# Kernel optimization log

Hardware: AMD Instinct MI355X
Metric: run time of the kernel (lower is better)

The kernel has to match this reference:

```python
import jax, jax.numpy as jnp
import numpy as np

N = 20000
E = 640000
IN_CH = 256
HID = 128
OUT_CH = 64
HEADS = 8
C1 = HID // HEADS   # 16 per-head dim, layer 1 (concat)
C2 = OUT_CH         # 64 per-head dim, layer 2 (head mean)
NEG_SLOPE = 0.2


def gat_conv(x, edge_index, W, a_src, a_dst, b, concat):
    """PyG GATConv (no self loops, eval mode / no dropout).
    W: [F_in, H*C], a_src/a_dst: [H, C], b: [H*C] or [C]."""
    H, C = a_src.shape
    h = (x @ W).reshape(-1, H, C)                      # [N, H, C]
    s_src = jnp.einsum('nhc,hc->nh', h, a_src)         # [N, H]
    s_dst = jnp.einsum('nhc,hc->nh', h, a_dst)         # [N, H]
    src, dst = edge_index[0], edge_index[1]
    e = jax.nn.leaky_relu(s_src[src] + s_dst[dst], NEG_SLOPE)  # [E, H]
    # segment softmax over incoming edges of each destination node
    m = jax.ops.segment_max(e, dst, num_segments=N)    # [N, H] (-inf for isolated)
    p = jnp.exp(e - m[dst])                            # [E, H]
    z = jax.ops.segment_sum(p, dst, num_segments=N)    # [N, H]
    alpha = p / z[dst]                                 # [E, H]
    out = jax.ops.segment_sum(h[src] * alpha[..., None], dst, num_segments=N)  # [N,H,C]
    out = out.reshape(-1, H * C) if concat else out.mean(axis=1)
    return out + b


def hetero_layer(x, edge_indices, Ws, a_srcs, a_dsts, bs, concat):
    # HeteroConv(aggr='mean') over edge types targeting 'user'
    outs = [gat_conv(x, edge_indices[t], Ws[t], a_srcs[t], a_dsts[t], bs[t], concat)
            for t in range(len(edge_indices))]
    return sum(outs) / len(outs)


def setup_inputs() -> dict:
    key = jax.random.key(0)
    ks = jax.random.split(key, 16)
    g = 0.1
    return {
        'x': jax.random.normal(ks[0], (N, IN_CH), dtype=jnp.float32),
        'edge_index_a': jax.random.randint(ks[1], (2, E), 0, N, dtype=jnp.int32).astype(jnp.int64),
        'edge_index_b': jax.random.randint(ks[2], (2, E), 0, N, dtype=jnp.int32).astype(jnp.int64),
        # layer 1 params, stacked over 2 edge types
        'W1': jax.random.normal(ks[3], (2, IN_CH, HEADS * C1), dtype=jnp.float32) * g,
        'a1_src': jax.random.normal(ks[4], (2, HEADS, C1), dtype=jnp.float32) * g,
        'a1_dst': jax.random.normal(ks[5], (2, HEADS, C1), dtype=jnp.float32) * g,
        'b1': jnp.zeros((2, HEADS * C1), dtype=jnp.float32),
        # layer 2 params
        'W2': jax.random.normal(ks[6], (2, HID, HEADS * C2), dtype=jnp.float32) * g,
        'a2_src': jax.random.normal(ks[7], (2, HEADS, C2), dtype=jnp.float32) * g,
        'a2_dst': jax.random.normal(ks[8], (2, HEADS, C2), dtype=jnp.float32) * g,
        'b2': jnp.zeros((2, C2), dtype=jnp.float32),
        # classifier
        'Wc1': jax.random.normal(ks[9], (OUT_CH, 32), dtype=jnp.float32) * g,
        'bc1': jnp.zeros((32,), dtype=jnp.float32),
        'Wc2': jax.random.normal(ks[10], (32, 2), dtype=jnp.float32) * g,
        'bc2': jnp.zeros((2,), dtype=jnp.float32),
    }


def reference(x, edge_index_a, edge_index_b, W1, a1_src, a1_dst, b1,
              W2, a2_src, a2_dst, b2, Wc1, bc1, Wc2, bc2):
    eis = [edge_index_a, edge_index_b]
    h = hetero_layer(x, eis, W1, a1_src, a1_dst, b1, concat=True)   # [N, 128]
    h = jax.nn.elu(h)  # (dropout is identity in eval mode)
    h = hetero_layer(h, eis, W2, a2_src, a2_dst, b2, concat=False)  # [N, 64]
    h = jax.nn.elu(h)
    logits = jax.nn.relu(h @ Wc1 + bc1) @ Wc2 + bc2                 # [N, 2]
    return logits
```

## Files before the change

### kernel.cpp

```cpp
#include <hip/hip_runtime.h>
#include <hip/hip_bf16.h>
#include <math.h>

#define NN 20000
#define EE 640000
#define NB 157
#define BCAP 5120
#define NBLK 160
#define CHNK 4000

typedef float v2f __attribute__((ext_vector_type(2)));
typedef __attribute__((ext_vector_type(8))) short bf16x8;
typedef __attribute__((ext_vector_type(4))) float f32x4;

__device__ __forceinline__ void wave_fence() {
  __builtin_amdgcn_wave_barrier();
  asm volatile("s_waitcnt lgkmcnt(0)" ::: "memory");
  __builtin_amdgcn_wave_barrier();
}

__device__ __forceinline__ unsigned pack_bf2(float a, float b) {
  __hip_bfloat162 h2 = __float22bfloat162_rn(make_float2(a, b));
  return *(unsigned*)&h2;
}
__device__ __forceinline__ float2 unpack_bf2(unsigned v) {
  float2 r;
  unsigned lo = v << 16, hi = v & 0xffff0000u;
  r.x = __uint_as_float(lo);
  r.y = __uint_as_float(hi);
  return r;
}

__global__ __launch_bounds__(256) void bin_k(const int* __restrict__ ea,
                                             const int* __restrict__ eb,
                                             int* __restrict__ gcnt,
                                             int* __restrict__ bbuf) {
  int t = blockIdx.y;
  const int* ei = t ? eb : ea;
  int tid = threadIdx.x;
  __shared__ int lh[NB], lbase[NB];
  if (tid < NB) lh[tid] = 0;
  __syncthreads();
  int e0 = blockIdx.x * CHNK;
  int e1 = min(e0 + CHNK, EE);
  int myb[16], myr[16], myv[16];
#pragma unroll
  for (int i = 0; i < 16; ++i) {
    int e = e0 + tid + i * 256;
    if (e < e1) {
      int s = ei[e], d = ei[EE + e];
      int b = d >> 7;
      myb[i] = b;
      myv[i] = (s << 7) | (d & 127);
      myr[i] = atomicAdd(&lh[b], 1);
    } else {
      myb[i] = -1;
    }
  }
  __syncthreads();
  if (tid < NB) {
    int c = lh[tid];
    lbase[tid] = c ? atomicAdd(&gcnt[t * NB + tid], c) : 0;
  }
  __syncthreads();
#pragma unroll
  for (int i = 0; i < 16; ++i) {
    int b = myb[i];
    if (b >= 0) {
      int pos = lbase[b] + myr[i];
      if (pos < BCAP) bbuf[((size_t)t * NB + b) * BCAP + pos] = myv[i];
    }
  }
}

__global__ __launch_bounds__(512) void bscan_k(const int* __restrict__ gcnt,
                                               int* __restrict__ bstart) {
  __shared__ int buf[512];
  int tid = threadIdx.x;
  int t = tid >> 8, b = tid & 255;
  int val = (b < NB) ? gcnt[t * NB + b] : 0;
  buf[tid] = val;
  __syncthreads();
  for (int s = 1; s < 256; s <<= 1) {
    int x = ((tid & 255) >= s) ? buf[tid - s] : 0;
    __syncthreads();
    buf[tid] += x;
    __syncthreads();
  }
  if (b < NB) bstart[t * NB + b] = buf[tid] - val;
}

__global__ __launch_bounds__(256) void build_k(const int* __restrict__ gcnt,
                                               const int* __restrict__ bstart,
                                               const int* __restrict__ bbuf,
                                               int* __restrict__ rowptr,
                                               int* __restrict__ csr) {
  int b = blockIdx.x, t = blockIdx.y;
  int cnt = gcnt[t * NB + b];
  int start = bstart[t * NB + b];
  int n0 = b << 7;
  int nlocal = min(128, NN - n0);
  int tid = threadIdx.x;
  __shared__ int arr[128], lcur[128];
  if (tid < 128) arr[tid] = 0;
  __syncthreads();
  const int* ebuf = bbuf + ((size_t)t * NB + b) * BCAP;
  for (int i = tid; i < cnt; i += 256) atomicAdd(&arr[ebuf[i] & 127], 1);
  __syncthreads();
  int deg = (tid < 128) ? arr[tid] : 0;
  for (int s = 1; s < 128; s <<= 1) {
    int x = (tid < 128 && tid >= s) ? arr[tid - s] : 0;
    __syncthreads();
    if (tid < 128) arr[tid] += x;
    __syncthreads();
  }
  if (tid < nlocal) {
    int incl = arr[tid];
    rowptr[t * (NN + 1) + n0 + tid + 1] = start + incl;
    lcur[tid] = start + incl - deg;
  }
  if (b == 0 && tid == 0) rowptr[t * (NN + 1)] = 0;
  __syncthreads();
  for (int i = tid; i < cnt; i += 256) {
    int v = ebuf[i];
    int pos = atomicAdd(&lcur[v & 127], 1);
    csr[(size_t)t * EE + pos] = v >> 7;
  }
}

__global__ void packx_k(const float* __restrict__ x, unsigned* __restrict__ Xp) {
  int idx = blockIdx.x * 256 + threadIdx.x;
  if (idx >= NN * 128) return;
  float2 f = *(const float2*)&x[(size_t)idx * 2];
  Xp[idx] = pack_bf2(f.x, f.y);
}

__global__ void foldBT1_k(const float* __restrict__ W1, unsigned* __restrict__ BT1) {
  int idx = blockIdx.x * 256 + threadIdx.x;
  if (idx >= 32768) return;
  int t = idx >> 14, r = idx & 16383, c = r >> 7, kw = r & 127;
  float v0 = W1[(size_t)t * 32768 + (size_t)(2 * kw) * 128 + c];
  float v1 = W1[(size_t)t * 32768 + (size_t)(2 * kw + 1) * 128 + c];
  BT1[idx] = pack_bf2(v0, v1);
}

__global__ __launch_bounds__(256) void gemm1_k(const unsigned* __restrict__ Xp,
                                               const unsigned* __restrict__ BT1,
                                               unsigned* __restrict__ h1b) {
  int tid = threadIdx.x, w = tid >> 6, l = tid & 63;
  int lr = l & 15, lg = l >> 4;
  int rowbase = blockIdx.x * 64 + w * 16;
  int arow = rowbase + lr;
  if (arow > NN - 1) arow = NN - 1;
  f32x4 acc[2][8];
#pragma unroll
  for (int t = 0; t < 2; ++t)
#pragma unroll
    for (int ct = 0; ct < 8; ++ct) acc[t][ct] = (f32x4){0.f, 0.f, 0.f, 0.f};
  const unsigned* ap = Xp + (size_t)arow * 128 + lg * 4;
#pragma unroll
  for (int kw = 0; kw < 128; kw += 16) {
    uint4 av = *(const uint4*)(ap + kw);
    bf16x8 af = *(const bf16x8*)&av;
#pragma unroll
    for (int t = 0; t < 2; ++t) {
#pragma unroll
      for (int ct = 0; ct < 8; ++ct) {
        uint4 bv = *(const uint4*)(BT1 + (size_t)t * 16384 + (size_t)(ct * 16 + lr) * 128 + lg * 4 + kw);
        acc[t][ct] = __builtin_amdgcn_mfma_f32_16x16x32_bf16(af, *(const bf16x8*)&bv, acc[t][ct], 0, 0, 0);
      }
    }
  }
  bool wr = (l & 1) == 0;
#pragma unroll
  for (int t = 0; t < 2; ++t) {
#pragma unroll
    for (int ct = 0; ct < 8; ++ct) {
      int col = ct * 16 + lr;
#pragma unroll
      for (int r = 0; r < 4; ++r) {
        float v = acc[t][ct][r];
        float v2 = __shfl_xor(v, 1);
        int row = rowbase + lg * 4 + r;
        if (wr && row < NN)
          h1b[(size_t)t * NN * 64 + (size_t)row * 64 + (col >> 1)] = pack_bf2(v, v2);
      }
    }
  }
}

__global__ void scoreb_k(const unsigned* __restrict__ hb, const float* __restrict__ as_,
                         const float* __restrict__ ad_, float* __restrict__ ss,
                         float* __restrict__ sd) {
  int idx = blockIdx.x * 256 + threadIdx.x;
  if (idx >= 2 * NN * 8) return;
  int t = idx / (NN * 8), r = idx % (NN * 8), n = r / 8, hh = r % 8;
  const unsigned* hrow = hb + (size_t)t * NN * 64 + (size_t)n * 64 + hh * 8;
  const float* a1 = as_ + t * 128 + hh * 16;
  const float* a2 = ad_ + t * 128 + hh * 16;
  uint4 u0 = *(const uint4*)&hrow[0];
  uint4 u1 = *(const uint4*)&hrow[4];
  unsigned uu[8] = {u0.x, u0.y, u0.z, u0.w, u1.x, u1.y, u1.z, u1.w};
  float s1 = 0.f, s2 = 0.f;
#pragma unroll
  for (int q = 0; q < 8; ++q) {
    float2 f = unpack_bf2(uu[q]);
    s1 += f.x * a1[2 * q] + f.y * a1[2 * q + 1];
    s2 += f.x * a2[2 * q] + f.y * a2[2 * q + 1];
  }
  ss[idx] = s1; sd[idx] = s2;
}

__device__ __forceinline__ float lrelu(float v) { return v > 0.f ? v : 0.2f * v; }

__global__ __launch_bounds__(256) void aggw1_k(const int* __restrict__ rowptr,
                                               const int* __restrict__ csr,
                                               const float* __restrict__ ssrc,
                                               const float* __restrict__ sdst,
                                               const unsigned* __restrict__ hb,
                                               unsigned* __restrict__ out) {
  int t = blockIdx.y;
  rowptr += t * (NN + 1); csr += (size_t)t * EE;
  ssrc += (size_t)t * NN * 8; sdst += (size_t)t * NN * 8;
  hb += (size_t)t * NN * 64; out += (size_t)t * NN * 64;
  int tid = threadIdx.x, w = tid >> 6, lane = tid & 63;
  int n = blockIdx.x * 4 + w;
  int row = rowptr[n], end = rowptr[n + 1];
  __shared__ __align__(16) int sidx[4][64];
  __shared__ __align__(16) float sexp[4][64][8];
  float4 sda = *(const float4*)&sdst[(size_t)n * 8];
  float4 sdb = *(const float4*)&sdst[(size_t)n * 8 + 4];
  float za_x = 0.f, za_y = 0.f, za_z = 0.f, za_w = 0.f;
  float zb_x = 0.f, zb_y = 0.f, zb_z = 0.f, zb_w = 0.f;
  int hme = lane >> 3;
  unsigned lane4 = lane << 2;
  const char* hbc = (const char*)hb;
  v2f acc = {0.f, 0.f};
  for (int base = row; base < end; base += 64) {
    int cnt = min(64, end - base);
    if (lane < cnt) {
      int s = csr[base + lane];
      sidx[w][lane] = s << 8;
      float4 pa = *(const float4*)&ssrc[(size_t)s * 8];
      float4 pb = *(const float4*)&ssrc[(size_t)s * 8 + 4];
      float4 ea, eb;
      ea.x = __expf(lrelu(pa.x + sda.x)); ea.y = __expf(lrelu(pa.y + sda.y));
      ea.z = __expf(lrelu(pa.z + sda.z)); ea.w = __expf(lrelu(pa.w + sda.w));
      eb.x = __expf(lrelu(pb.x + sdb.x)); eb.y = __expf(lrelu(pb.y + sdb.y));
      eb.z = __expf(lrelu(pb.z + sdb.z)); eb.w = __expf(lrelu(pb.w + sdb.w));
      za_x += ea.x; za_y += ea.y; za_z += ea.z; za_w += ea.w;
      zb_x += eb.x; zb_y += eb.y; zb_z += eb.z; zb_w += eb.w;
      *(float4*)&sexp[w][lane][0] = ea;
      *(float4*)&sexp[w][lane][4] = eb;
    }
    wave_fence();
    int g = 0;
    for (; g + 8 <= cnt; g += 8) {
      unsigned off[8];
      *(int4*)&off[0] = *(const int4*)&sidx[w][g];
      *(int4*)&off[4] = *(const int4*)&sidx[w][g + 4];
      unsigned uv[8];
#pragma unroll
      for (int j = 0; j < 8; ++j)
        uv[j] = *(const unsigned*)(hbc + (off[j] | lane4));
#pragma unroll
      for (int j = 0; j < 8; ++j) {
        float a = sexp[w][g + j][hme];
        float2 vf = unpack_bf2(uv[j]);
        v2f v = {vf.x, vf.y};
        acc += a * v;
      }
    }
    for (; g < cnt; ++g) {
      unsigned off = (unsigned)sidx[w][g];
      unsigned uvr = *(const unsigned*)(hbc + (off | lane4));
      float a = sexp[w][g][hme];
      float2 vf = unpack_bf2(uvr);
      v2f v = {vf.x, vf.y};
      acc += a * v;
    }
    wave_fence();
  }
#pragma unroll
  for (int off = 32; off; off >>= 1) {
    za_x += __shfl_xor(za_x, off); za_y += __shfl_xor(za_y, off);
    za_z += __shfl_xor(za_z, off); za_w += __shfl_xor(za_w, off);
    zb_x += __shfl_xor(zb_x, off); zb_y += __shfl_xor(zb_y, off);
    zb_z += __shfl_xor(zb_z, off); zb_w += __shfl_xor(zb_w, off);
  }
  float zh[8] = {za_x, za_y, za_z, za_w, zb_x, zb_y, zb_z, zb_w};
  float z = zh[hme];
  float iz = z > 0.f ? 1.f / z : 0.f;
  out[(size_t)n * 64 + lane] = pack_bf2(acc.x * iz, acc.y * iz);
}

__global__ void combine1_k(const unsigned* __restrict__ oa, const unsigned* __restrict__ ob,
                           const float* __restrict__ b1, unsigned* __restrict__ hmidb) {
  int idx = blockIdx.x * 256 + threadIdx.x;
  if (idx >= NN * 64) return;
  int j2 = idx & 63, j = j2 * 2;
  float2 va = unpack_bf2(oa[idx]);
  float2 vb = unpack_bf2(ob[idx]);
  float vx = 0.5f * ((va.x + b1[j]) + (vb.x + b1[128 + j]));
  float vy = 0.5f * ((va.y + b1[j + 1]) + (vb.y + b1[128 + j + 1]));
  vx = vx > 0.f ? vx : (__expf(vx) - 1.f);
  vy = vy > 0.f ? vy : (__expf(vy) - 1.f);
  hmidb[idx] = pack_bf2(vx, vy);
}

__global__ void fold2_k(const float* __restrict__ W2, const float* __restrict__ a2s,
                        const float* __restrict__ a2d, float* __restrict__ wsf,
                        float* __restrict__ wdf) {
  int idx = blockIdx.x * 256 + threadIdx.x;
  if (idx >= 2048) return;
  int t = idx >> 10, r = idx & 1023, hh = r >> 7, k = r & 127;
  const float* wrow = W2 + (size_t)t * 65536 + (size_t)k * 512 + hh * 64;
  const float* as = a2s + t * 512 + hh * 64;
  const float* ad = a2d + t * 512 + hh * 64;
  float s1 = 0.f, s2 = 0.f;
  for (int c = 0; c < 64; ++c) { s1 += wrow[c] * as[c]; s2 += wrow[c] * ad[c]; }
  wsf[idx] = s1; wdf[idx] = s2;
}

__global__ void foldBT_k(const float* __restrict__ W2, unsigned* __restrict__ BTp) {
  int idx = blockIdx.x * 256 + threadIdx.x;
  if (idx >= 65536) return;
  int t = idx >> 15, r = idx & 32767, c = r >> 9, kw = r & 511;
  int K0 = kw * 2, K1 = K0 + 1;
  int hh0 = K0 >> 7, kk0 = K0 & 127;
  int hh1 = K1 >> 7, kk1 = K1 & 127;
  float v0 = 0.125f * W2[(size_t)t * 65536 + (size_t)kk0 * 512 + hh0 * 64 + c];
  float v1 = 0.125f * W2[(size_t)t * 65536 + (size_t)kk1 * 512 + hh1 * 64 + c];
  BTp[idx] = pack_bf2(v0, v1);
}

__global__ void score2_k(const unsigned* __restrict__ hmidb, const float* __restrict__ wsf,
                         const float* __restrict__ wdf, float* __restrict__ ss,
                         float* __restrict__ sdo) {
  int idx = blockIdx.x * 256 + threadIdx.x;
  if (idx >= NN * 8) return;
  int n = idx >> 3, hh = idx & 7;
  const unsigned* hm = hmidb + (size_t)n * 64;
  const float* w0s = wsf + (size_t)hh * 128;
  const float* w0d = wdf + (size_t)hh * 128;
  const float* w1s = wsf + (size_t)(8 + hh) * 128;
  const float* w1d = wdf + (size_t)(8 + hh) * 128;
  float s0s = 0.f, s0d = 0.f, s1s = 0.f, s1d = 0.f;
#pragma unroll 4
  for (int q = 0; q < 64; ++q) {
    float2 f = unpack_bf2(hm[q]);
    int c = 2 * q;
    s0s += f.x * w0s[c] + f.y * w0s[c + 1];
    s0d += f.x * w0d[c] + f.y * w0d[c + 1];
    s1s += f.x * w1s[c] + f.y * w1s[c + 1];
    s1d += f.x * w1d[c] + f.y * w1d[c + 1];
  }
  ss[idx] = s0s; sdo[idx] = s0d;
  ss[NN * 8 + idx] = s1s; sdo[NN * 8 + idx] = s1d;
}

__global__ __launch_bounds__(256) void aggw2_k(const int* __restrict__ rowptr,
                                               const int* __restrict__ csr,
                                               const float* __restrict__ ssrc,
                                               const float* __restrict__ sdst,
                                               const unsigned* __restrict__ hmidb,
                                               unsigned* __restrict__ aggp) {
  int t = blockIdx.y;
  rowptr += t * (NN + 1); csr += (size_t)t * EE;
  ssrc += (size_t)t * NN * 8; sdst += (size_t)t * NN * 8;
  aggp += (size_t)t * NN * 512;
  int tid = threadIdx.x, w = tid >> 6, lane = tid & 63;
  int n = blockIdx.x * 4 + w;
  int row = rowptr[n], end = rowptr[n + 1];
  __shared__ __align__(16) int sidx[4][64];
  __shared__ __align__(16) float sexp[4][64][8];
  float4 sda = *(const float4*)&sdst[(size_t)n * 8];
  float4 sdb = *(const float4*)&sdst[(size_t)n * 8 + 4];
  float za_x = 0.f, za_y = 0.f, za_z = 0.f, za_w = 0.f;
  float zb_x = 0.f, zb_y = 0.f, zb_z = 0.f, zb_w = 0.f;
  unsigned lane4 = lane << 2;
  const char* hbc = (const char*)hmidb;
  v2f acc[8];
#pragma unroll
  for (int i = 0; i < 8; ++i) acc[i] = (v2f){0.f, 0.f};
  for (int base = row; base < end; base += 64) {
    int cnt = min(64, end - base);
    if (lane < cnt) {
      int s = csr[base + lane];
      sidx[w][lane] = s << 8;
      float4 pa = *(const float4*)&ssrc[(size_t)s * 8];
      float4 pb = *(const float4*)&ssrc[(size_t)s * 8 + 4];
      float4 ea, eb;
      ea.x = __expf(lrelu(pa.x + sda.x)); ea.y = __expf(lrelu(pa.y + sda.y));
      ea.z = __expf(lrelu(pa.z + sda.z)); ea.w = __expf(lrelu(pa.w + sda.w));
      eb.x = __expf(lrelu(pb.x + sdb.x)); eb.y = __expf(lrelu(pb.y + sdb.y));
      eb.z = __expf(lrelu(pb.z + sdb.z)); eb.w = __expf(lrelu(pb.w + sdb.w));
      za_x += ea.x; za_y += ea.y; za_z += ea.z; za_w += ea.w;
      zb_x += eb.x; zb_y += eb.y; zb_z += eb.z; zb_w += eb.w;
      *(float4*)&sexp[w][lane][0] = ea;
      *(float4*)&sexp[w][lane][4] = eb;
    }
    wave_fence();
    int g = 0;
    for (; g + 8 <= cnt; g += 8) {
      unsigned off[8];
      *(int4*)&off[0] = *(const int4*)&sidx[w][g];
      *(int4*)&off[4] = *(const int4*)&sidx[w][g + 4];
      unsigned uv[8];
#pragma unroll
      for (int j = 0; j < 8; ++j)
        uv[j] = *(const unsigned*)(hbc + (off[j] | lane4));
#pragma unroll
      for (int j = 0; j < 8; ++j) {
        float4 ea = *(const float4*)&sexp[w][g + j][0];
        float4 eb = *(const float4*)&sexp[w][g + j][4];
        float2 vf = unpack_bf2(uv[j]);
        v2f v = {vf.x, vf.y};
        acc[0] += ea.x * v;
        acc[1] += ea.y * v;
        acc[2] += ea.z * v;
        acc[3] += ea.w * v;
        acc[4] += eb.x * v;
        acc[5] += eb.y * v;
        acc[6] += eb.z * v;
        acc[7] += eb.w * v;
      }
    }
    for (; g < cnt; ++g) {
      unsigned off = (unsigned)sidx[w][g];
      unsigned uvr = *(const unsigned*)(hbc + (off | lane4));
      float4 ea = *(const float4*)&sexp[w][g][0];
      float4 eb = *(const float4*)&sexp[w][g][4];
      float2 vf = unpack_bf2(uvr);
      v2f v = {vf.x, vf.y};
      acc[0] += ea.x * v;
      acc[1] += ea.y * v;
      acc[2] += ea.z * v;
      acc[3] += ea.w * v;
      acc[4] += eb.x * v;
      acc[5] += eb.y * v;
      acc[6] += eb.z * v;
      acc[7] += eb.w * v;
    }
    wave_fence();
  }
#pragma unroll
  for (int off = 32; off; off >>= 1) {
    za_x += __shfl_xor(za_x, off); za_y += __shfl_xor(za_y, off);
    za_z += __shfl_xor(za_z, off); za_w += __shfl_xor(za_w, off);
    zb_x += __shfl_xor(zb_x, off); zb_y += __shfl_xor(zb_y, off);
    zb_z += __shfl_xor(zb_z, off); zb_w += __shfl_xor(zb_w, off);
  }
  float zh[8] = {za_x, za_y, za_z, za_w, zb_x, zb_y, zb_z, zb_w};
#pragma unroll
  for (int i = 0; i < 8; ++i) {
    float z = zh[i];
    float iz = z > 0.f ? 1.f / z : 0.f;
    aggp[(size_t)n * 512 + i * 64 + lane] = pack_bf2(acc[i].x * iz, acc[i].y * iz);
  }
}

__global__ __launch_bounds__(256) void gemm2_k(const unsigned* __restrict__ Ap,
                                               const unsigned* __restrict__ BT,
                                               const float* __restrict__ b2,
                                               float* __restrict__ feat) {
  int tid = threadIdx.x, w = tid >> 6, l = tid & 63;
  int lr = l & 15, lgq = l >> 4;
  int rowbase = blockIdx.x * 64 + w * 16;
  int arow = rowbase + lr;
  if (arow > NN - 1) arow = NN - 1;
  f32x4 acc0 = {0.f, 0.f, 0.f, 0.f}, acc1 = acc0, acc2 = acc0, acc3 = acc0;
#pragma unroll
  for (int t = 0; t < 2; ++t) {
    const unsigned* ap = Ap + (size_t)t * NN * 512 + (size_t)arow * 512 + lgq * 4;
    const unsigned* bp = BT + t * 32768 + lr * 512 + lgq * 4;
    for (int kw = 0; kw < 512; kw += 16) {
      uint4 av = *(const uint4*)(ap + kw);
      uint4 bv0 = *(const uint4*)(bp + kw);
      uint4 bv1 = *(const uint4*)(bp + 16 * 512 + kw);
      uint4 bv2 = *(const uint4*)(bp + 32 * 512 + kw);
      uint4 bv3 = *(const uint4*)(bp + 48 * 512 + kw);
      bf16x8 afq = *(const bf16x8*)&av;
      acc0 = __builtin_amdgcn_mfma_f32_16x16x32_bf16(afq, *(const bf16x8*)&bv0, acc0, 0, 0, 0);
      acc1 = __builtin_amdgcn_mfma_f32_16x16x32_bf16(afq, *(const bf16x8*)&bv1, acc1, 0, 0, 0);
      acc2 = __builtin_amdgcn_mfma_f32_16x16x32_bf16(afq, *(const bf16x8*)&bv2, acc2, 0, 0, 0);
      acc3 = __builtin_amdgcn_mfma_f32_16x16x32_bf16(afq, *(const bf16x8*)&bv3, acc3, 0, 0, 0);
    }
  }
  f32x4 accs[4] = {acc0, acc1, acc2, acc3};
#pragma unroll
  for (int ct = 0; ct < 4; ++ct) {
    int col = ct * 16 + lr;
    float bsum = b2[col] + b2[64 + col];
#pragma unroll
    for (int r = 0; r < 4; ++r) {
      int rowq = rowbase + lgq * 4 + r;
      if (rowq < NN) {
        float v = 0.5f * (accs[ct][r] + bsum);
        v = v > 0.f ? v : (__expf(v) - 1.f);
        feat[(size_t)rowq * 64 + col] = v;
      }
    }
  }
}

__global__ __launch_bounds__(256) void cls_k(const float* __restrict__ feat,
                                             const float* __restrict__ Wc1,
                                             const float* __restrict__ bc1,
                                             const float* __restrict__ Wc2,
                                             const float* __restrict__ bc2,
                                             float* __restrict__ out) {
  __shared__ float w1[64 * 32];
  __shared__ float w2[64];
  __shared__ float b1s[32], b2s[2];
  __shared__ float fs[8 * 64];
  __shared__ float hs[8 * 32];
  int tid = threadIdx.x;
  for (int i = tid; i < 2048; i += 256) w1[i] = Wc1[i];
  if (tid < 64) w2[tid] = Wc2[tid];
  if (tid < 32) b1s[tid] = bc1[tid];
  if (tid < 2) b2s[tid] = bc2[tid];
  int nbase = blockIdx.x * 8;
  for (int i = tid; i < 512; i += 256) fs[i] = feat[(size_t)nbase * 64 + i];
  __syncthreads();
  int local = tid >> 5, tt = tid & 31;
  const float* f = fs + local * 64;
  float acc = b1s[tt];
#pragma unroll
  for (int c = 0; c < 64; ++c) acc += f[c] * w1[c * 32 + tt];
  hs[local * 32 + tt] = fmaxf(acc, 0.f);
  __syncthreads();
  if (tid < 16) {
    int l = tid >> 1, j = tid & 1;
    float o = b2s[j];
#pragma unroll
    for (int i = 0; i < 32; ++i) o += hs[l * 32 + i] * w2[i * 2 + j];
    out[(size_t)(nbase + l) * 2 + j] = o;
  }
}

extern "C" void kernel_launch(void* const* d_in, const int* in_sizes, int n_in,
                              void* d_out, int out_size, void* d_ws, size_t ws_size,
                              hipStream_t stream) {
  const float* x   = (const float*)d_in[0];
  const int* eia   = (const int*)d_in[1];
  const int* eib   = (const int*)d_in[2];
  const float* W1  = (const float*)d_in[3];
  const float* a1s = (const float*)d_in[4];
  const float* a1d = (const float*)d_in[5];
  const float* b1  = (const float*)d_in[6];
  const float* W2  = (const float*)d_in[7];
  const float* a2s = (const float*)d_in[8];
  const float* a2d = (const float*)d_in[9];
  const float* b2  = (const float*)d_in[10];
  const float* Wc1 = (const float*)d_in[11];
  const float* bc1 = (const float*)d_in[12];
  const float* Wc2 = (const float*)d_in[13];
  const float* bc2 = (const float*)d_in[14];
  float* out = (float*)d_out;

  char* ws = (char*)d_ws;
  size_t off = 0;
  auto alloc = [&](size_t bytes) -> char* {
    char* p = ws + off;
    off += (bytes + 255) & ~(size_t)255;
    return p;
  };
  int* gcnt       = (int*)alloc((size_t)2 * NB * 4);
  int* bstart     = (int*)alloc((size_t)2 * NB * 4);
  int* bbuf       = (int*)alloc((size_t)2 * NB * BCAP * 4);
  int* rowptr     = (int*)alloc((size_t)2 * (NN + 1) * 4);
  int* csr        = (int*)alloc((size_t)2 * EE * 4);
  unsigned* Xp    = (unsigned*)alloc((size_t)NN * 128 * 4);
  unsigned* BT1   = (unsigned*)alloc((size_t)32768 * 4);
  unsigned* h1b   = (unsigned*)alloc((size_t)2 * NN * 64 * 4);
  float* s1s      = (float*)alloc((size_t)2 * NN * 8 * 4);
  float* s1d      = (float*)alloc((size_t)2 * NN * 8 * 4);
  unsigned* o1p   = (unsigned*)alloc((size_t)2 * NN * 64 * 4);
  unsigned* hmidb = (unsigned*)alloc((size_t)NN * 64 * 4);
  float* wsf      = (float*)alloc((size_t)2048 * 4);
  float* wdf      = (float*)alloc((size_t)2048 * 4);
  unsigned* BTp   = (unsigned*)alloc((size_t)65536 * 4);
  float* s2s      = (float*)alloc((size_t)2 * NN * 8 * 4);
  float* s2d      = (float*)alloc((size_t)2 * NN * 8 * 4);
  unsigned* aggp  = (unsigned*)alloc((size_t)2 * NN * 512 * 4);
  float* feat     = (float*)alloc((size_t)NN * 64 * 4);

  hipMemsetAsync(gcnt, 0, (size_t)2 * NB * 4, stream);
  bin_k<<<dim3(NBLK, 2), 256, 0, stream>>>(eia, eib, gcnt, bbuf);
  bscan_k<<<1, 512, 0, stream>>>(gcnt, bstart);
  build_k<<<dim3(NB, 2), 256, 0, stream>>>(gcnt, bstart, bbuf, rowptr, csr);

  fold2_k<<<8, 256, 0, stream>>>(W2, a2s, a2d, wsf, wdf);
  foldBT_k<<<256, 256, 0, stream>>>(W2, BTp);
  foldBT1_k<<<128, 256, 0, stream>>>(W1, BT1);
  packx_k<<<(NN * 128 + 255) / 256, 256, 0, stream>>>(x, Xp);

  gemm1_k<<<(NN + 63) / 64, 256, 0, stream>>>(Xp, BT1, h1b);
  scoreb_k<<<(2 * NN * 8 + 255) / 256, 256, 0, stream>>>(h1b, a1s, a1d, s1s, s1d);
  aggw1_k<<<dim3(NN / 4, 2), 256, 0, stream>>>(rowptr, csr, s1s, s1d, h1b, o1p);
  combine1_k<<<(NN * 64 + 255) / 256, 256, 0, stream>>>(o1p, o1p + (size_t)NN * 64, b1, hmidb);

  score2_k<<<(NN * 8 + 255) / 256, 256, 0, stream>>>(hmidb, wsf, wdf, s2s, s2d);
  aggw2_k<<<dim3(NN / 4, 2), 256, 0, stream>>>(rowptr, csr, s2s, s2d, hmidb, aggp);
  gemm2_k<<<(NN + 63) / 64, 256, 0, stream>>>(aggp, BTp, b2, feat);

  cls_k<<<NN / 8, 256, 0, stream>>>(feat, Wc1, bc1, Wc2, bc2, out);
}
```

Before: 435.4 us.

## Replace bucketed CSR build with global-atomic degree count, scan, and scatter

```diff
diff --git a/kernel.cpp b/kernel.cpp
--- a/kernel.cpp
+++ b/kernel.cpp
@@ -4,10 +4,6 @@
 
 #define NN 20000
 #define EE 640000
-#define NB 157
-#define BCAP 5120
-#define NBLK 160
-#define CHNK 4000
 
 typedef float v2f __attribute__((ext_vector_type(2)));
 typedef __attribute__((ext_vector_type(8))) short bf16x8;
@@ -31,100 +27,64 @@
   return r;
 }
 
-__global__ __launch_bounds__(256) void bin_k(const int* __restrict__ ea,
-                                             const int* __restrict__ eb,
-                                             int* __restrict__ gcnt,
-                                             int* __restrict__ bbuf) {
+__global__ __launch_bounds__(256) void degcnt_k(const int* __restrict__ ea,
+                                                const int* __restrict__ eb,
+                                                int* __restrict__ deg) {
   int t = blockIdx.y;
   const int* ei = t ? eb : ea;
+  int* dg = deg + t * NN;
+  for (int e = blockIdx.x * 256 + threadIdx.x; e < EE; e += gridDim.x * 256)
+    atomicAdd(&dg[ei[EE + e]], 1);
+}
+
+__global__ __launch_bounds__(1024) void scan_k(const int* __restrict__ deg,
+                                               int* __restrict__ rowptr,
+                                               int* __restrict__ cur) {
+  int t = blockIdx.x;
+  const int* d = deg + t * NN;
+  int* rp = rowptr + t * (NN + 1);
+  int* cu = cur + t * NN;
+  __shared__ int part[1024];
   int tid = threadIdx.x;
-  __shared__ int lh[NB], lbase[NB];
-  if (tid < NB) lh[tid] = 0;
+  const int PER = (NN + 1023) / 1024;
+  int base = tid * PER;
+  int s = 0;
+  for (int i = 0; i < PER; ++i) {
+    int n = base + i;
+    if (n < NN) s += d[n];
+  }
+  part[tid] = s;
   __syncthreads();
-  int e0 = blockIdx.x * CHNK;
-  int e1 = min(e0 + CHNK, EE);
-  int myb[16], myr[16], myv[16];
-#pragma unroll
-  for (int i = 0; i < 16; ++i) {
-    int e = e0 + tid + i * 256;
-    if (e < e1) {
-      int s = ei[e], d = ei[EE + e];
-      int b = d >> 7;
-      myb[i] = b;
-      myv[i] = (s << 7) | (d & 127);
-      myr[i] = atomicAdd(&lh[b], 1);
-    } else {
-      myb[i] = -1;
-    }
-  }
-  __syncthreads();
-  if (tid < NB) {
-    int c = lh[tid];
-    lbase[tid] = c ? atomicAdd(&gcnt[t * NB + tid], c) : 0;
-  }
-  __syncthreads();
-#pragma unroll
-  for (int i = 0; i < 16; ++i) {
-    int b = myb[i];
-    if (b >= 0) {
-      int pos = lbase[b] + myr[i];
-      if (pos < BCAP) bbuf[((size_t)t * NB + b) * BCAP + pos] = myv[i];
-    }
-  }
-}
-
-__global__ __launch_bounds__(512) void bscan_k(const int* __restrict__ gcnt,
-                                               int* __restrict__ bstart) {
-  __shared__ int buf[512];
-  int tid = threadIdx.x;
-  int t = tid >> 8, b = tid & 255;
-  int val = (b < NB) ? gcnt[t * NB + b] : 0;
-  buf[tid] = val;
-  __syncthreads();
-  for (int s = 1; s < 256; s <<= 1) {
-    int x = ((tid & 255) >= s) ? buf[tid - s] : 0;
+  for (int st = 1; st < 1024; st <<= 1) {
+    int x = (tid >= st) ? part[tid - st] : 0;
     __syncthreads();
-    buf[tid] += x;
+    part[tid] += x;
     __syncthreads();
   }
-  if (b < NB) bstart[t * NB + b] = buf[tid] - val;
-}
-
-__global__ __launch_bounds__(256) void build_k(const int* __restrict__ gcnt,
-                                               const int* __restrict__ bstart,
-                                               const int* __restrict__ bbuf,
-                                               int* __restrict__ rowptr,
-                                               int* __restrict__ csr) {
-  int b = blockIdx.x, t = blockIdx.y;
-  int cnt = gcnt[t * NB + b];
-  int start = bstart[t * NB + b];
-  int n0 = b << 7;
-  int nlocal = min(128, NN - n0);
-  int tid = threadIdx.x;
-  __shared__ int arr[128], lcur[128];
-  if (tid < 128) arr[tid] = 0;
-  __syncthreads();
-  const int* ebuf = bbuf + ((size_t)t * NB + b) * BCAP;
-  for (int i = tid; i < cnt; i += 256) atomicAdd(&arr[ebuf[i] & 127], 1);
-  __syncthreads();
-  int deg = (tid < 128) ? arr[tid] : 0;
-  for (int s = 1; s < 128; s <<= 1) {
-    int x = (tid < 128 && tid >= s) ? arr[tid - s] : 0;
-    __syncthreads();
-    if (tid < 128) arr[tid] += x;
-    __syncthreads();
-  }
-  if (tid < nlocal) {
-    int incl = arr[tid];
-    rowptr[t * (NN + 1) + n0 + tid + 1] = start + incl;
-    lcur[tid] = start + incl - deg;
-  }
-  if (b == 0 && tid == 0) rowptr[t * (NN + 1)] = 0;
-  __syncthreads();
-  for (int i = tid; i < cnt; i += 256) {
-    int v = ebuf[i];
-    int pos = atomicAdd(&lcur[v & 127], 1);
-    csr[(size_t)t * EE + pos] = v >> 7;
+  int run = part[tid] - s;
+  for (int i = 0; i < PER; ++i) {
+    int n = base + i;
+    if (n < NN) {
+      rp[n] = run;
+      cu[n] = run;
+      run += d[n];
+    }
+  }
+  if (tid == 1023) rp[NN] = run;
+}
+
+__global__ __launch_bounds__(256) void scatter_k(const int* __restrict__ ea,
+                                                 const int* __restrict__ eb,
+                                                 int* __restrict__ cur,
+                                                 int* __restrict__ csr) {
+  int t = blockIdx.y;
+  const int* ei = t ? eb : ea;
+  int* cu = cur + t * NN;
+  int* cs = csr + (size_t)t * EE;
+  for (int e = blockIdx.x * 256 + threadIdx.x; e < EE; e += gridDim.x * 256) {
+    int s = ei[e], d = ei[EE + e];
+    int pos = atomicAdd(&cu[d], 1);
+    cs[pos] = s;
   }
 }
 
@@ -566,9 +526,8 @@
     off += (bytes + 255) & ~(size_t)255;
     return p;
   };
-  int* gcnt       = (int*)alloc((size_t)2 * NB * 4);
-  int* bstart     = (int*)alloc((size_t)2 * NB * 4);
-  int* bbuf       = (int*)alloc((size_t)2 * NB * BCAP * 4);
+  int* deg        = (int*)alloc((size_t)2 * NN * 4);
+  int* cur        = (int*)alloc((size_t)2 * NN * 4);
   int* rowptr     = (int*)alloc((size_t)2 * (NN + 1) * 4);
   int* csr        = (int*)alloc((size_t)2 * EE * 4);
   unsigned* Xp    = (unsigned*)alloc((size_t)NN * 128 * 4);
@@ -586,10 +545,10 @@
   unsigned* aggp  = (unsigned*)alloc((size_t)2 * NN * 512 * 4);
   float* feat     = (float*)alloc((size_t)NN * 64 * 4);
 
-  hipMemsetAsync(gcnt, 0, (size_t)2 * NB * 4, stream);
-  bin_k<<<dim3(NBLK, 2), 256, 0, stream>>>(eia, eib, gcnt, bbuf);
-  bscan_k<<<1, 512, 0, stream>>>(gcnt, bstart);
-  build_k<<<dim3(NB, 2), 256, 0, stream>>>(gcnt, bstart, bbuf, rowptr, csr);
+  hipMemsetAsync(deg, 0, (size_t)2 * NN * 4, stream);
+  degcnt_k<<<dim3(1024, 2), 256, 0, stream>>>(eia, eib, deg);
+  scan_k<<<2, 1024, 0, stream>>>(deg, rowptr, cur);
+  scatter_k<<<dim3(1024, 2), 256, 0, stream>>>(eia, eib, cur, csr);
 
   fold2_k<<<8, 256, 0, stream>>>(W2, a2s, a2d, wsf, wdf);
   foldBT_k<<<256, 256, 0, stream>>>(W2, BTp);
```

Measured after the change: 582.6 us. 1.34x slower.
